# Optimization experiments

Measured on AMD Instinct MI355X. Metric: run time of the kernel, lower is better.

Reference implementation:

```python
import jax, jax.numpy as jnp
import numpy as np

N_NODES = 50000
N_EDGES = 600000
DIMS = [1280, 512, 300, 300]


def setup_inputs() -> dict:
    key = jax.random.key(0)
    ks = jax.random.split(key, 8)
    x = jax.random.normal(ks[0], (N_NODES, DIMS[0]), dtype=jnp.float32)
    edge_index = jax.random.randint(ks[1], (2, N_EDGES), 0, N_NODES, dtype=jnp.int64)
    def w(k, i, o):
        return jax.random.normal(k, (i, o), dtype=jnp.float32) * (1.0 / np.sqrt(i))
    W1 = w(ks[2], DIMS[0], DIMS[1]); b1 = jnp.zeros((DIMS[1],), jnp.float32)
    W2 = w(ks[3], DIMS[1], DIMS[2]); b2 = jnp.zeros((DIMS[2],), jnp.float32)
    W3 = w(ks[4], DIMS[2], DIMS[3]); b3 = jnp.zeros((DIMS[3],), jnp.float32)
    return {"x": x, "W1": W1, "b1": b1, "W2": W2, "b2": b2,
            "W3": W3, "b3": b3, "edge_index": edge_index}


def gcn_conv(x, W, b, src, dst, n):
    """PyG GCNConv: add self-loops, symmetric D^-1/2 (A+I) D^-1/2 aggregation."""
    h = x @ W  # [N, out]
    loops = jnp.arange(n, dtype=src.dtype)
    s = jnp.concatenate([src, loops])  # [E+N]
    d = jnp.concatenate([dst, loops])
    deg = jax.ops.segment_sum(jnp.ones_like(d, dtype=h.dtype), d, num_segments=n)
    dinv = jnp.where(deg > 0, jax.lax.rsqrt(deg), 0.0)
    norm = dinv[s] * dinv[d]  # [E+N]
    out = jax.ops.segment_sum(h[s] * norm[:, None], d, num_segments=n)
    return out + b


def reference(x, W1, b1, W2, b2, W3, b3, edge_index):
    src, dst = edge_index[0], edge_index[1]
    n = x.shape[0]
    # dropout is identity in eval mode; pertubed=False path
    h = jax.nn.relu(gcn_conv(x, W1, b1, src, dst, n))
    h = jax.nn.relu(gcn_conv(h, W2, b2, src, dst, n))
    h = jax.nn.relu(gcn_conv(h, W3, b3, src, dst, n))
    return h  # [N, 300]; per-graph split is a trivial mask over data.batch
```

## Files before the change

### kernel.cpp

```cpp
#include <hip/hip_runtime.h>

typedef _Float16 f16;
typedef _Float16 f16x2 __attribute__((ext_vector_type(2)));
typedef _Float16 f16x4 __attribute__((ext_vector_type(4)));
typedef _Float16 f16x8 __attribute__((ext_vector_type(8)));
typedef float f32x4 __attribute__((ext_vector_type(4)));

#define N_NODES 50000
#define N_EDGES 600000

__device__ __forceinline__ void gl_lds16(const void* g, void* l) {
  __builtin_amdgcn_global_load_lds(
      (__attribute__((address_space(1))) void*)(g),
      (__attribute__((address_space(3))) void*)(l), 16, 0, 0);
}

__global__ void k_setup(const float* __restrict__ x, f16* __restrict__ xh,
                        const float* __restrict__ W1, f16* __restrict__ w1h,
                        const float* __restrict__ W2, f16* __restrict__ w2h,
                        const float* __restrict__ W3, f16* __restrict__ w3h,
                        const float* __restrict__ b2, float* __restrict__ bp2,
                        const float* __restrict__ b3, float* __restrict__ bp3,
                        const int* __restrict__ edst, int* __restrict__ deg) {
  const int b = blockIdx.x, t = threadIdx.x;
  if (b < 62500) {
    long i = (long)b * 256 + t;
    float4 v = ((const float4*)x)[i];
    f16x4 o;
    o[0] = (f16)v.x; o[1] = (f16)v.y; o[2] = (f16)v.z; o[3] = (f16)v.w;
    ((f16x4*)xh)[i] = o;
  } else if (b < 64844) {
    int e = (b - 62500) * 256 + t;
    if (e < N_EDGES) atomicAdd(&deg[edst[e]], 1);
  } else if (b < 67404) {
    int idx = (b - 64844) * 256 + t;
    int n = idx / 1280, k = idx - n * 1280;
    w1h[idx] = (f16)W1[(size_t)k * 512 + n];
  } else if (b < 68004) {
    int bb = b - 67404;
    int n = bb >> 1, k = (bb & 1) * 256 + t;
    if (k < 512) w2h[(size_t)n * 512 + k] = (f16)W2[(size_t)k * 300 + n];
  } else if (b < 68604) {
    int bb = b - 68004;
    int n = bb >> 1, k = (bb & 1) * 256 + t;
    if (k < 320) w3h[(size_t)n * 320 + k] = (k < 300) ? (f16)W3[(size_t)k * 300 + n] : (f16)0.f;
  } else if (b < 68606) {
    int i = (b - 68604) * 256 + t;
    if (i < 320) bp2[i] = (i < 300) ? b2[i] : 0.f;
  } else {
    int i = (b - 68606) * 256 + t;
    if (i < 320) bp3[i] = (i < 300) ? b3[i] : 0.f;
  }
}

__device__ __forceinline__ int block_incl_scan256(int v, int t) {
  __shared__ int wsum[4];
  const int lane = t & 63, w = t >> 6;
  int incl = v;
#pragma unroll
  for (int off = 1; off < 64; off <<= 1) {
    int u = __shfl_up(incl, off, 64);
    if (lane >= off) incl += u;
  }
  if (lane == 63) wsum[w] = incl;
  __syncthreads();
  int add = 0;
#pragma unroll
  for (int k = 0; k < 4; ++k)
    if (k < w) add += wsum[k];
  return incl + add;
}

__global__ void k_scan1(const int* __restrict__ deg, float* __restrict__ dinv,
                        int* __restrict__ bsum, int n) {
  __shared__ int ws4[4];
  const int t = threadIdx.x, b = blockIdx.x;
  const int i = b * 256 + t;
  int v = (i < n) ? deg[i] : 0;
  if (i < n) dinv[i] = rsqrtf((float)(v + 1));
  int s = v;
#pragma unroll
  for (int off = 1; off < 64; off <<= 1) s += __shfl_xor(s, off, 64);
  if ((t & 63) == 0) ws4[t >> 6] = s;
  __syncthreads();
  if (t == 0) bsum[b] = ws4[0] + ws4[1] + ws4[2] + ws4[3];
}

__global__ void k_scan2(const int* __restrict__ bsum, int* __restrict__ bpre,
                        int* __restrict__ rowptr, int nb, int n) {
  const int t = threadIdx.x;
  int v = (t < nb) ? bsum[t] : 0;
  int incl = block_incl_scan256(v, t);
  if (t < nb) bpre[t] = incl - v;
  if (t == 255) rowptr[n] = incl;
}

__global__ void k_scan3(const int* __restrict__ deg, const int* __restrict__ bpre,
                        int* __restrict__ rowptr, int* __restrict__ rptr2, int n) {
  const int t = threadIdx.x, b = blockIdx.x;
  const int i = b * 256 + t;
  int v = (i < n) ? deg[i] : 0;
  int incl = block_incl_scan256(v, t);
  int ex = bpre[b] + incl - v;
  if (i < n) { rowptr[i] = ex; rptr2[i] = ex; }
}

__global__ void k_fill(const int* __restrict__ src, const int* __restrict__ dst,
                       int* __restrict__ rptr2, int2* __restrict__ meta,
                       const float* __restrict__ dinv, int E) {
  int e = blockIdx.x * 256 + threadIdx.x;
  if (e < E) {
    int d = dst[e], s = src[e];
    int pos = atomicAdd(&rptr2[d], 1);
    float w = dinv[s] * dinv[d];
    meta[pos] = make_int2(s, __float_as_int(w));
  }
}

__global__ __launch_bounds__(256, 3)
void gemm_f16_tn(const f16* __restrict__ A, const f16* __restrict__ B,
                 f16* __restrict__ C, int M, int N, int K,
                 int lda, int ldb, int ldc) {
  __shared__ __align__(16) f16 As[128 * 64];
  __shared__ __align__(16) f16 Bs[128 * 64];
  const int tid = threadIdx.x;
  const int wave = tid >> 6;
  const int lane = tid & 63;
  const int bm = blockIdx.y, bn = blockIdx.x;

  const int r8 = lane >> 3;
  const int sunit = (lane & 7) ^ r8;
  const char* aSrc[4];
  const char* bSrc[4];
#pragma unroll
  for (int c = 0; c < 4; ++c) {
    long ar = (long)bm * 128 + wave * 32 + c * 8 + r8; if (ar > M - 1) ar = M - 1;
    long br = (long)bn * 128 + wave * 32 + c * 8 + r8; if (br > N - 1) br = N - 1;
    aSrc[c] = (const char*)(A + ar * lda) + sunit * 16;
    bSrc[c] = (const char*)(B + br * ldb) + sunit * 16;
  }

  const int r16 = lane & 15;
  const int kq = lane >> 4;
  const int wm = wave & 1, wn = wave >> 1;

  int aoff[4][2], boff[4][2];
#pragma unroll
  for (int t = 0; t < 4; ++t) {
#pragma unroll
    for (int ks = 0; ks < 2; ++ks) {
      int arow = wm * 64 + t * 16 + r16;
      aoff[t][ks] = arow * 128 + ((((ks << 2) + kq) ^ (arow & 7)) << 4);
      int brow = wn * 64 + t * 16 + r16;
      boff[t][ks] = brow * 128 + ((((ks << 2) + kq) ^ (brow & 7)) << 4);
    }
  }

  f32x4 acc[4][4] = {};

  for (int k0 = 0; k0 < K; k0 += 64) {
    __syncthreads();
    const size_t kb = (size_t)k0 * 2;
#pragma unroll
    for (int c = 0; c < 4; ++c) {
      gl_lds16(aSrc[c] + kb, (char*)As + (wave * 32 + c * 8) * 128);
      gl_lds16(bSrc[c] + kb, (char*)Bs + (wave * 32 + c * 8) * 128);
    }
    __syncthreads();

#pragma unroll
    for (int ks = 0; ks < 2; ++ks) {
      f16x8 af[4], bf[4];
#pragma unroll
      for (int t = 0; t < 4; ++t) {
        af[t] = *(const f16x8*)((const char*)As + aoff[t][ks]);
        bf[t] = *(const f16x8*)((const char*)Bs + boff[t][ks]);
      }
#pragma unroll
      for (int mt = 0; mt < 4; ++mt)
#pragma unroll
        for (int nt = 0; nt < 4; ++nt)
          acc[mt][nt] = __builtin_amdgcn_mfma_f32_16x16x32_f16(af[mt], bf[nt], acc[mt][nt], 0, 0, 0);
    }
  }

  const int crow0 = bm * 128 + wm * 64;
  const int ccol0 = bn * 128 + wn * 64;
#pragma unroll
  for (int mt = 0; mt < 4; ++mt)
#pragma unroll
    for (int nt = 0; nt < 4; ++nt)
#pragma unroll
      for (int r = 0; r < 4; ++r) {
        int row = crow0 + mt * 16 + kq * 4 + r;
        int col = ccol0 + nt * 16 + r16;
        if (row < M && col < ldc)
          C[(size_t)row * ldc + col] = (col < N) ? (f16)acc[mt][nt][r] : (f16)0.f;
      }
}

template <int LDH, int ACT, bool F16OUT, int DOUT>
__global__ __launch_bounds__(256, 8)
void agg_relu3(const f16* __restrict__ h, const int* __restrict__ rowptr,
               const int2* __restrict__ meta, const float* __restrict__ dinv,
               const float* __restrict__ bias, void* __restrict__ outp, int nNodes) {
  const int tid = threadIdx.x;
  const int lane = tid & 63;
  const int node = blockIdx.x * 4 + (tid >> 6);
  if (node >= nNodes) return;
  const int r0 = __builtin_amdgcn_readfirstlane(rowptr[node]);
  const int r1 = __builtin_amdgcn_readfirstlane(rowptr[node + 1]);
  const float dv = __builtin_bit_cast(
      float, __builtin_amdgcn_readfirstlane(__builtin_bit_cast(int, dinv[node])));

  const int hoff = (lane < ACT ? lane : ACT - 1) * 8;
  const f16* hp = h + hoff;

  float acc[8];
  {
    f16x8 v = *(const f16x8*)(hp + (size_t)node * LDH);
    const float w0 = dv * dv;
#pragma unroll
    for (int j = 0; j < 8; ++j) acc[j] = w0 * (float)v[j];
  }

  for (int base = r0; base < r1; base += 64) {
    const int idx = base + lane;
    int2 m = (idx < r1) ? meta[idx] : make_int2(0, 0);
    const int cnt = min(64, r1 - base);
    int j = 0;
    for (; j + 2 <= cnt; j += 2) {
      int s0 = __shfl(m.x, j, 64);
      int s1 = __shfl(m.x, j + 1, 64);
      float w0 = __int_as_float(__shfl(m.y, j, 64));
      float w1 = __int_as_float(__shfl(m.y, j + 1, 64));
      f16x8 v0 = *(const f16x8*)(hp + (size_t)s0 * LDH);
      f16x8 v1 = *(const f16x8*)(hp + (size_t)s1 * LDH);
#pragma unroll
      for (int q = 0; q < 8; ++q) acc[q] = fmaf(w0, (float)v0[q], acc[q]);
#pragma unroll
      for (int q = 0; q < 8; ++q) acc[q] = fmaf(w1, (float)v1[q], acc[q]);
    }
    if (j < cnt) {
      int s0 = __shfl(m.x, j, 64);
      float w0 = __int_as_float(__shfl(m.y, j, 64));
      f16x8 v0 = *(const f16x8*)(hp + (size_t)s0 * LDH);
#pragma unroll
      for (int q = 0; q < 8; ++q) acc[q] = fmaf(w0, (float)v0[q], acc[q]);
    }
  }

  float4 bv0 = *(const float4*)(bias + hoff);
  float4 bv1 = *(const float4*)(bias + hoff + 4);
  float o[8];
  o[0] = fmaxf(acc[0] + bv0.x, 0.f); o[1] = fmaxf(acc[1] + bv0.y, 0.f);
  o[2] = fmaxf(acc[2] + bv0.z, 0.f); o[3] = fmaxf(acc[3] + bv0.w, 0.f);
  o[4] = fmaxf(acc[4] + bv1.x, 0.f); o[5] = fmaxf(acc[5] + bv1.y, 0.f);
  o[6] = fmaxf(acc[6] + bv1.z, 0.f); o[7] = fmaxf(acc[7] + bv1.w, 0.f);

  if constexpr (F16OUT) {
    if (lane < ACT) {
      f16x8 ov;
#pragma unroll
      for (int j = 0; j < 8; ++j) ov[j] = (f16)o[j];
      *(f16x8*)((f16*)outp + (size_t)node * LDH + lane * 8) = ov;
    }
  } else {
    float* orow = (float*)outp + (size_t)node * DOUT + lane * 8;
    if (lane * 8 + 4 <= DOUT)
      *(float4*)(orow) = make_float4(o[0], o[1], o[2], o[3]);
    if (lane * 8 + 8 <= DOUT)
      *(float4*)(orow + 4) = make_float4(o[4], o[5], o[6], o[7]);
  }
}

extern "C" void kernel_launch(void* const* d_in, const int* in_sizes, int n_in,
                              void* d_out, int out_size, void* d_ws, size_t ws_size,
                              hipStream_t stream) {
  const float* x  = (const float*)d_in[0];
  const float* W1 = (const float*)d_in[1];
  const float* b1 = (const float*)d_in[2];
  const float* W2 = (const float*)d_in[3];
  const float* b2 = (const float*)d_in[4];
  const float* W3 = (const float*)d_in[5];
  const float* b3 = (const float*)d_in[6];
  const int* eidx = (const int*)d_in[7];
  const int* esrc = eidx;
  const int* edst = eidx + N_EDGES;
  float* out = (float*)d_out;

  char* ws = (char*)d_ws;
  f16* xh = (f16*)(ws);
  f16* h2 = (f16*)(ws);
  f16* g2 = (f16*)(ws + 32000000);
  f16* h3 = (f16*)(ws + 64000000);
  f16* h1 = (f16*)(ws + 128000000);
  f16* g1 = (f16*)(ws + 179200000);
  f16* w1h = (f16*)(ws + 230400000);
  f16* w2h = (f16*)(ws + 231710720);
  f16* w3h = (f16*)(ws + 232017920);
  float* bp2 = (float*)(ws + 232209920);
  float* bp3 = (float*)(ws + 232211200);
  int* deg    = (int*)(ws + 232212480);
  float* dinv = (float*)(ws + 232412480);
  int* rowptr = (int*)(ws + 232612480);
  int* rptr2  = (int*)(ws + 232812484);
  int* bsum   = (int*)(ws + 233012488);
  int* bpre   = (int*)(ws + 233013288);
  int2* meta  = (int2*)(ws + 233014088);

  hipMemsetAsync(deg, 0, N_NODES * sizeof(int), stream);

  k_setup<<<68608, 256, 0, stream>>>(x, xh, W1, w1h, W2, w2h, W3, w3h,
                                     b2, bp2, b3, bp3, edst, deg);

  k_scan1<<<196, 256, 0, stream>>>(deg, dinv, bsum, N_NODES);
  k_scan2<<<1, 256, 0, stream>>>(bsum, bpre, rowptr, 196, N_NODES);
  k_scan3<<<196, 256, 0, stream>>>(deg, bpre, rowptr, rptr2, N_NODES);
  k_fill<<<2344, 256, 0, stream>>>(esrc, edst, rptr2, meta, dinv, N_EDGES);

  gemm_f16_tn<<<dim3(4, 391), 256, 0, stream>>>(xh, w1h, h1, N_NODES, 512, 1280, 1280, 1280, 512);
  agg_relu3<512, 64, true, 0><<<12500, 256, 0, stream>>>(h1, rowptr, meta, dinv, b1, g1, N_NODES);

  gemm_f16_tn<<<dim3(3, 391), 256, 0, stream>>>(g1, w2h, h2, N_NODES, 300, 512, 512, 512, 320);
  agg_relu3<320, 40, true, 0><<<12500, 256, 0, stream>>>(h2, rowptr, meta, dinv, bp2, g2, N_NODES);

  gemm_f16_tn<<<dim3(3, 391), 256, 0, stream>>>(g2, w3h, h3, N_NODES, 300, 320, 320, 320, 320);
  agg_relu3<320, 38, false, 300><<<12500, 256, 0, stream>>>(h3, rowptr, meta, dinv, bp3, out, N_NODES);
}
```

Before: 795.4 us.

## Fuse fp32-to-fp16 input conversion into first GEMM's LDS load path

Drops the standalone pass that converts x from fp32 to fp16 and adds a GEMM variant that loads fp32 A tiles into LDS and converts them to fp16 in registers before the MFMAs. This removes one full read and write of the large input activation and a big chunk of the setup kernel. In exchange each column block now re-reads fp32 rows (twice the bytes per tile), LDS use per block grows, and extra conversion instructions sit in the inner loop.

```diff
diff --git a/kernel.cpp b/kernel.cpp
--- a/kernel.cpp
+++ b/kernel.cpp
@@ -15,40 +15,33 @@
       (__attribute__((address_space(3))) void*)(l), 16, 0, 0);
 }
 
-__global__ void k_setup(const float* __restrict__ x, f16* __restrict__ xh,
-                        const float* __restrict__ W1, f16* __restrict__ w1h,
+__global__ void k_setup(const float* __restrict__ W1, f16* __restrict__ w1h,
                         const float* __restrict__ W2, f16* __restrict__ w2h,
                         const float* __restrict__ W3, f16* __restrict__ w3h,
                         const float* __restrict__ b2, float* __restrict__ bp2,
                         const float* __restrict__ b3, float* __restrict__ bp3,
                         const int* __restrict__ edst, int* __restrict__ deg) {
   const int b = blockIdx.x, t = threadIdx.x;
-  if (b < 62500) {
-    long i = (long)b * 256 + t;
-    float4 v = ((const float4*)x)[i];
-    f16x4 o;
-    o[0] = (f16)v.x; o[1] = (f16)v.y; o[2] = (f16)v.z; o[3] = (f16)v.w;
-    ((f16x4*)xh)[i] = o;
-  } else if (b < 64844) {
-    int e = (b - 62500) * 256 + t;
+  if (b < 2344) {
+    int e = b * 256 + t;
     if (e < N_EDGES) atomicAdd(&deg[edst[e]], 1);
-  } else if (b < 67404) {
-    int idx = (b - 64844) * 256 + t;
+  } else if (b < 4904) {
+    int idx = (b - 2344) * 256 + t;
     int n = idx / 1280, k = idx - n * 1280;
     w1h[idx] = (f16)W1[(size_t)k * 512 + n];
-  } else if (b < 68004) {
-    int bb = b - 67404;
+  } else if (b < 5504) {
+    int bb = b - 4904;
     int n = bb >> 1, k = (bb & 1) * 256 + t;
     if (k < 512) w2h[(size_t)n * 512 + k] = (f16)W2[(size_t)k * 300 + n];
-  } else if (b < 68604) {
-    int bb = b - 68004;
+  } else if (b < 6104) {
+    int bb = b - 5504;
     int n = bb >> 1, k = (bb & 1) * 256 + t;
     if (k < 320) w3h[(size_t)n * 320 + k] = (k < 300) ? (f16)W3[(size_t)k * 300 + n] : (f16)0.f;
-  } else if (b < 68606) {
-    int i = (b - 68604) * 256 + t;
+  } else if (b < 6106) {
+    int i = (b - 6104) * 256 + t;
     if (i < 320) bp2[i] = (i < 300) ? b2[i] : 0.f;
   } else {
-    int i = (b - 68606) * 256 + t;
+    int i = (b - 6106) * 256 + t;
     if (i < 320) bp3[i] = (i < 300) ? b3[i] : 0.f;
   }
 }
@@ -174,6 +167,106 @@
 #pragma unroll
       for (int t = 0; t < 4; ++t) {
         af[t] = *(const f16x8*)((const char*)As + aoff[t][ks]);
+        bf[t] = *(const f16x8*)((const char*)Bs + boff[t][ks]);
+      }
+#pragma unroll
+      for (int mt = 0; mt < 4; ++mt)
+#pragma unroll
+        for (int nt = 0; nt < 4; ++nt)
+          acc[mt][nt] = __builtin_amdgcn_mfma_f32_16x16x32_f16(af[mt], bf[nt], acc[mt][nt], 0, 0, 0);
+    }
+  }
+
+  const int crow0 = bm * 128 + wm * 64;
+  const int ccol0 = bn * 128 + wn * 64;
+#pragma unroll
+  for (int mt = 0; mt < 4; ++mt)
+#pragma unroll
+    for (int nt = 0; nt < 4; ++nt)
+#pragma unroll
+      for (int r = 0; r < 4; ++r) {
+        int row = crow0 + mt * 16 + kq * 4 + r;
+        int col = ccol0 + nt * 16 + r16;
+        if (row < M && col < ldc)
+          C[(size_t)row * ldc + col] = (col < N) ? (f16)acc[mt][nt][r] : (f16)0.f;
+      }
+}
+
+__global__ __launch_bounds__(256, 3)
+void gemm_f32a_tn(const float* __restrict__ A, const f16* __restrict__ B,
+                  f16* __restrict__ C, int M, int N, int K,
+                  int lda, int ldb, int ldc) {
+  __shared__ __align__(16) float As[128 * 64];
+  __shared__ __align__(16) f16 Bs[128 * 64];
+  const int tid = threadIdx.x;
+  const int wave = tid >> 6;
+  const int lane = tid & 63;
+  const int bm = blockIdx.y, bn = blockIdx.x;
+
+  const int r8 = lane >> 3;
+  const int bunit = (lane & 7) ^ r8;
+  const char* bSrc[4];
+#pragma unroll
+  for (int c = 0; c < 4; ++c) {
+    long br = (long)bn * 128 + wave * 32 + c * 8 + r8; if (br > N - 1) br = N - 1;
+    bSrc[c] = (const char*)(B + br * ldb) + bunit * 16;
+  }
+
+  const int arow4 = lane >> 4;
+  const int u16 = lane & 15;
+  const int u32h = u16 & 1;
+  const char* aSrc[8];
+#pragma unroll
+  for (int c = 0; c < 8; ++c) {
+    int row_lo = c * 4 + arow4;
+    long ar = (long)bm * 128 + wave * 32 + row_lo; if (ar > M - 1) ar = M - 1;
+    int s3 = row_lo & 7;
+    int srcoff = (((u16 >> 1) ^ s3) << 5) + (u32h << 4);
+    aSrc[c] = (const char*)(A + ar * lda) + srcoff;
+  }
+
+  const int r16 = lane & 15;
+  const int kq = lane >> 4;
+  const int wm = wave & 1, wn = wave >> 1;
+
+  int aoff[4][2], boff[4][2];
+#pragma unroll
+  for (int t = 0; t < 4; ++t) {
+#pragma unroll
+    for (int ks = 0; ks < 2; ++ks) {
+      int arow = wm * 64 + t * 16 + r16;
+      aoff[t][ks] = arow * 256 + ((((ks << 2) + kq) ^ (arow & 7)) << 5);
+      int brow = wn * 64 + t * 16 + r16;
+      boff[t][ks] = brow * 128 + ((((ks << 2) + kq) ^ (brow & 7)) << 4);
+    }
+  }
+
+  f32x4 acc[4][4] = {};
+
+  for (int k0 = 0; k0 < K; k0 += 64) {
+    __syncthreads();
+    const size_t kbA = (size_t)k0 * 4;
+    const size_t kbB = (size_t)k0 * 2;
+#pragma unroll
+    for (int c = 0; c < 4; ++c)
+      gl_lds16(bSrc[c] + kbB, (char*)Bs + (wave * 32 + c * 8) * 128);
+#pragma unroll
+    for (int c = 0; c < 8; ++c)
+      gl_lds16(aSrc[c] + kbA, (char*)As + (wave * 32 + c * 4) * 256);
+    __syncthreads();
+
+#pragma unroll
+    for (int ks = 0; ks < 2; ++ks) {
+      f16x8 af[4], bf[4];
+#pragma unroll
+      for (int t = 0; t < 4; ++t) {
+        const char* ap = (const char*)As + aoff[t][ks];
+        f32x4 lo = *(const f32x4*)(ap);
+        f32x4 hi = *(const f32x4*)(ap + 16);
+        f16x8 a;
+        a[0] = (f16)lo[0]; a[1] = (f16)lo[1]; a[2] = (f16)lo[2]; a[3] = (f16)lo[3];
+        a[4] = (f16)hi[0]; a[5] = (f16)hi[1]; a[6] = (f16)hi[2]; a[7] = (f16)hi[3];
+        af[t] = a;
         bf[t] = *(const f16x8*)((const char*)Bs + boff[t][ks]);
       }
 #pragma unroll
@@ -290,7 +383,6 @@
   float* out = (float*)d_out;
 
   char* ws = (char*)d_ws;
-  f16* xh = (f16*)(ws);
   f16* h2 = (f16*)(ws);
   f16* g2 = (f16*)(ws + 32000000);
   f16* h3 = (f16*)(ws + 64000000);
@@ -311,15 +403,15 @@
 
   hipMemsetAsync(deg, 0, N_NODES * sizeof(int), stream);
 
-  k_setup<<<68608, 256, 0, stream>>>(x, xh, W1, w1h, W2, w2h, W3, w3h,
-                                     b2, bp2, b3, bp3, edst, deg);
+  k_setup<<<6108, 256, 0, stream>>>(W1, w1h, W2, w2h, W3, w3h,
+                                    b2, bp2, b3, bp3, edst, deg);
 
   k_scan1<<<196, 256, 0, stream>>>(deg, dinv, bsum, N_NODES);
   k_scan2<<<1, 256, 0, stream>>>(bsum, bpre, rowptr, 196, N_NODES);
   k_scan3<<<196, 256, 0, stream>>>(deg, bpre, rowptr, rptr2, N_NODES);
   k_fill<<<2344, 256, 0, stream>>>(esrc, edst, rptr2, meta, dinv, N_EDGES);
 
-  gemm_f16_tn<<<dim3(4, 391), 256, 0, stream>>>(xh, w1h, h1, N_NODES, 512, 1280, 1280, 1280, 512);
+  gemm_f32a_tn<<<dim3(4, 391), 256, 0, stream>>>(x, w1h, h1, N_NODES, 512, 1280, 1280, 1280, 512);
   agg_relu3<512, 64, true, 0><<<12500, 256, 0, stream>>>(h1, rowptr, meta, dinv, b1, g1, N_NODES);
 
   gemm_f16_tn<<<dim3(3, 391), 256, 0, stream>>>(g1, w2h, h2, N_NODES, 300, 512, 512, 512, 320);
```

Result: no change. 797.3 us (+0.2%).
